# Kernel optimization log

Hardware: AMD Instinct MI355X
Metric: run time of the kernel (lower is better)

Reference implementation:

```python
import jax, jax.numpy as jnp
import numpy as np

N = 50000
E = 800000
D_IN = 128
D_HID = 128
D_OUT = 64
BN_EPS = 1e-5


def setup_inputs() -> dict:
    key = jax.random.key(0)
    ks = jax.random.split(key, 16)
    s = lambda k, shp, fan: jax.random.normal(k, shp, dtype=jnp.float32) / np.sqrt(fan)
    return {
        "x": jax.random.normal(ks[0], (N, D_IN), dtype=jnp.float32),
        "edge_index": jax.random.randint(ks[1], (2, E), 0, N, dtype=jnp.int64),
        # layer 1: SAGEConv(in -> hid)
        "w1l": s(ks[2], (D_IN, D_HID), D_IN),
        "w1r": s(ks[3], (D_IN, D_HID), D_IN),
        "b1": jnp.zeros((D_HID,), jnp.float32),
        "g1": jnp.ones((D_HID,), jnp.float32),
        "be1": jnp.zeros((D_HID,), jnp.float32),
        # layer 2: SAGEConv(hid -> hid)
        "w2l": s(ks[4], (D_HID, D_HID), D_HID),
        "w2r": s(ks[5], (D_HID, D_HID), D_HID),
        "b2": jnp.zeros((D_HID,), jnp.float32),
        "g2": jnp.ones((D_HID,), jnp.float32),
        "be2": jnp.zeros((D_HID,), jnp.float32),
        # layer 3: SAGEConv(hid -> out)
        "w3l": s(ks[6], (D_HID, D_OUT), D_HID),
        "w3r": s(ks[7], (D_HID, D_OUT), D_HID),
        "b3": jnp.zeros((D_OUT,), jnp.float32),
    }


def sage_conv(x, src, dst, wl, wr, b):
    # mean aggregation of source-node features onto destination nodes
    msg_sum = jax.ops.segment_sum(x[src], dst, num_segments=N)  # [N, d]
    deg = jax.ops.segment_sum(jnp.ones((src.shape[0],), x.dtype), dst, num_segments=N)
    mean = msg_sum / jnp.maximum(deg, 1.0)[:, None]
    return mean @ wl + x @ wr + b


def batch_norm(x, g, b):
    mu = jnp.mean(x, axis=0)
    var = jnp.var(x, axis=0)
    return (x - mu) * jax.lax.rsqrt(var + BN_EPS) * g + b


def reference(x, edge_index, w1l, w1r, b1, g1, be1, w2l, w2r, b2, g2, be2, w3l, w3r, b3):
    src, dst = edge_index[0], edge_index[1]
    h = sage_conv(x, src, dst, w1l, w1r, b1)
    h = jax.nn.relu(batch_norm(h, g1, be1))
    h = sage_conv(h, src, dst, w2l, w2r, b2)
    h = jax.nn.relu(batch_norm(h, g2, be2))
    return sage_conv(h, src, dst, w3l, w3r, b3)
```

## Files before the change

### kernel.cpp

```cpp
#include <hip/hip_runtime.h>
#include <hip/hip_bf16.h>

#define NN 50000
#define NE 800000
#define DH 128
#define NB1 196
#define NBK 391
#define EPB 4096

typedef __attribute__((ext_vector_type(8))) short bf16x8;
typedef __attribute__((ext_vector_type(4))) float f32x4;
typedef __attribute__((ext_vector_type(8))) unsigned short us8;
typedef __attribute__((ext_vector_type(4))) unsigned short us4;

__device__ __forceinline__ unsigned short f2bf(float f) {
  unsigned int u = __builtin_bit_cast(unsigned int, f);
  unsigned int r = (u + 0x7FFFu + ((u >> 16) & 1u)) >> 16;
  return (unsigned short)r;
}
__device__ __forceinline__ float bf2f(unsigned int h16) {
  unsigned int u = h16 << 16;
  return __builtin_bit_cast(float, u);
}

__global__ void k_cvt_x(const float* __restrict__ x, unsigned short* __restrict__ xb, int n8) {
  int i = blockIdx.x * blockDim.x + threadIdx.x;
  if (i >= n8) return;
  const float4* p = reinterpret_cast<const float4*>(x) + (size_t)i * 2;
  float4 a = p[0], b = p[1];
  us8 o;
  o[0] = f2bf(a.x); o[1] = f2bf(a.y); o[2] = f2bf(a.z); o[3] = f2bf(a.w);
  o[4] = f2bf(b.x); o[5] = f2bf(b.y); o[6] = f2bf(b.z); o[7] = f2bf(b.w);
  reinterpret_cast<us8*>(xb)[i] = o;
}

__global__ void k_prep_w(const float* __restrict__ wl, const float* __restrict__ wr,
                         unsigned short* __restrict__ wt, int dout) {
  int idx = blockIdx.x * blockDim.x + threadIdx.x;
  if (idx >= dout * 256) return;
  int c = idx >> 8, k = idx & 255;
  float v = (k < DH) ? wl[k * dout + c] : wr[(k - DH) * dout + c];
  wt[idx] = f2bf(v);
}

__global__ void k_prep_w3(const float* __restrict__ w3l, const float* __restrict__ w3r,
                          unsigned short* __restrict__ wt) {
  int idx = blockIdx.x * blockDim.x + threadIdx.x;
  if (idx >= 128 * 128) return;
  int c = idx >> 7, k = idx & 127;
  float v = (c < 64) ? w3l[k * 64 + c] : w3r[k * 64 + (c - 64)];
  wt[idx] = f2bf(v);
}

__global__ void k_deg(const int* __restrict__ dst, int* __restrict__ deg) {
  int e = blockIdx.x * blockDim.x + threadIdx.x;
  if (e < NE) atomicAdd(&deg[dst[e]], 1);
}

__global__ void k_scan1(const int* __restrict__ deg, int* __restrict__ iscan,
                        int* __restrict__ bsum) {
  __shared__ int s[256];
  int t = threadIdx.x;
  int i = blockIdx.x * 256 + t;
  int d = (i < NN) ? deg[i] : 0;
  s[t] = d;
  __syncthreads();
  for (int off = 1; off < 256; off <<= 1) {
    int v = (t >= off) ? s[t - off] : 0;
    __syncthreads();
    s[t] += v;
    __syncthreads();
  }
  if (i < NN) iscan[i] = s[t];
  if (t == 255) bsum[blockIdx.x] = s[255];
}

__global__ void k_scan2(int* __restrict__ bsum) {
  __shared__ int s[256];
  int t = threadIdx.x;
  int v = (t < NB1) ? bsum[t] : 0;
  s[t] = v;
  __syncthreads();
  for (int off = 1; off < 256; off <<= 1) {
    int u = (t >= off) ? s[t - off] : 0;
    __syncthreads();
    s[t] += u;
    __syncthreads();
  }
  if (t < NB1) bsum[t] = s[t] - v;
}

__global__ void k_scan3(const int* __restrict__ deg, const int* __restrict__ iscan,
                        const int* __restrict__ bsum, int* __restrict__ rowptr,
                        int* __restrict__ bcursor, float* __restrict__ invd) {
  int i = blockIdx.x * 256 + threadIdx.x;
  if (i >= NN) return;
  int d = deg[i];
  int excl = bsum[blockIdx.x] + iscan[i] - d;
  rowptr[i] = excl;
  if ((i & 127) == 0) bcursor[i >> 7] = excl;
  invd[i] = 1.0f / (float)(d > 0 ? d : 1);
  if (i == 0) rowptr[NN] = NE;
}

__global__ __launch_bounds__(256) void k_bucket(const int* __restrict__ src,
                                                const int* __restrict__ dst,
                                                int* __restrict__ bcursor,
                                                int2* __restrict__ ebuf) {
  __shared__ int lcnt[NBK], lbase[NBK];
  int t = threadIdx.x;
  for (int b = t; b < NBK; b += 256) lcnt[b] = 0;
  __syncthreads();
  int base = blockIdx.x * EPB;
  int d[16], s[16];
#pragma unroll
  for (int i = 0; i < 16; ++i) {
    int e = base + i * 256 + t;
    if (e < NE) { d[i] = dst[e]; s[i] = src[e]; }
    else d[i] = -1;
  }
#pragma unroll
  for (int i = 0; i < 16; ++i)
    if (d[i] >= 0) atomicAdd(&lcnt[d[i] >> 7], 1);
  __syncthreads();
  for (int b = t; b < NBK; b += 256) {
    int c = lcnt[b];
    lbase[b] = c > 0 ? atomicAdd(&bcursor[b], c) : 0;
    lcnt[b] = 0;
  }
  __syncthreads();
#pragma unroll
  for (int i = 0; i < 16; ++i) {
    if (d[i] >= 0) {
      int b = d[i] >> 7;
      int r = atomicAdd(&lcnt[b], 1);
      ebuf[lbase[b] + r] = make_int2(s[i], d[i]);
    }
  }
}

__global__ __launch_bounds__(256) void k_fill2(const int* __restrict__ rowptr,
                                               const int2* __restrict__ ebuf,
                                               int* __restrict__ adj) {
  int b = blockIdx.x;
  int n0 = b << 7;
  int n1 = n0 + 128; if (n1 > NN) n1 = NN;
  __shared__ int cur[128];
  int t = threadIdx.x;
  if (t < n1 - n0) cur[t] = rowptr[n0 + t];
  __syncthreads();
  int e0 = rowptr[n0], e1 = rowptr[n1];
  for (int e = e0 + t; e < e1; e += 256) {
    int2 pr = ebuf[e];
    int p = atomicAdd(&cur[pr.y - n0], 1);
    adj[p] = pr.x;
  }
}

__global__ __launch_bounds__(256) void k_agg(const unsigned short* __restrict__ h,
                                             const int* __restrict__ rowptr,
                                             const int* __restrict__ adj,
                                             const float* __restrict__ invd,
                                             unsigned short* __restrict__ meanb) {
  int wid = (blockIdx.x * blockDim.x + threadIdx.x) >> 6;
  int lane = threadIdx.x & 63;
  if (wid >= NN) return;
  int lo = rowptr[wid], hi = rowptr[wid + 1];
  int q = lane >> 4;
  int c = (lane & 15) << 3;
  float a[8] = {};
  int e = lo;
#pragma unroll 2
  for (; e + 4 <= hi; e += 4) {
    int s = adj[e + q];
    us8 v = *reinterpret_cast<const us8*>(h + (size_t)s * DH + c);
#pragma unroll
    for (int j = 0; j < 8; ++j) a[j] += bf2f(v[j]);
  }
  if (q < hi - e) {
    int s = adj[e + q];
    us8 v = *reinterpret_cast<const us8*>(h + (size_t)s * DH + c);
#pragma unroll
    for (int j = 0; j < 8; ++j) a[j] += bf2f(v[j]);
  }
#pragma unroll
  for (int j = 0; j < 8; ++j) {
    a[j] += __shfl_xor(a[j], 16);
    a[j] += __shfl_xor(a[j], 32);
  }
  if (q == 0) {
    float iv = invd[wid];
    us8 o;
#pragma unroll
    for (int j = 0; j < 8; ++j) o[j] = f2bf(a[j] * iv);
    *reinterpret_cast<us8*>(meanb + (size_t)wid * DH + c) = o;
  }
}

__global__ __launch_bounds__(256) void k_agg3(const unsigned short* __restrict__ t3,
                                              const int* __restrict__ rowptr,
                                              const int* __restrict__ adj,
                                              const float* __restrict__ invd,
                                              const float* __restrict__ b3,
                                              float* __restrict__ out) {
  int wid = (blockIdx.x * blockDim.x + threadIdx.x) >> 6;
  int lane = threadIdx.x & 63;
  if (wid >= NN) return;
  int lo = rowptr[wid], hi = rowptr[wid + 1];
  int q = lane >> 4;
  int c = (lane & 15) << 2;
  float a[4] = {};
  int e = lo;
#pragma unroll 2
  for (; e + 4 <= hi; e += 4) {
    int s = adj[e + q];
    us4 v = *reinterpret_cast<const us4*>(t3 + (size_t)s * 128 + c);
#pragma unroll
    for (int j = 0; j < 4; ++j) a[j] += bf2f(v[j]);
  }
  if (q < hi - e) {
    int s = adj[e + q];
    us4 v = *reinterpret_cast<const us4*>(t3 + (size_t)s * 128 + c);
#pragma unroll
    for (int j = 0; j < 4; ++j) a[j] += bf2f(v[j]);
  }
#pragma unroll
  for (int j = 0; j < 4; ++j) {
    a[j] += __shfl_xor(a[j], 16);
    a[j] += __shfl_xor(a[j], 32);
  }
  if (q == 0) {
    float iv = invd[wid];
    us4 w = *reinterpret_cast<const us4*>(t3 + (size_t)wid * 128 + 64 + c);
    float4 o;
    o.x = a[0] * iv + bf2f(w[0]) + b3[c + 0];
    o.y = a[1] * iv + bf2f(w[1]) + b3[c + 1];
    o.z = a[2] * iv + bf2f(w[2]) + b3[c + 2];
    o.w = a[3] * iv + bf2f(w[3]) + b3[c + 3];
    *reinterpret_cast<float4*>(out + (size_t)wid * 64 + c) = o;
  }
}

template <bool SPLIT, bool STATS>
__global__ __launch_bounds__(256) void k_gemm(const unsigned short* __restrict__ Am,
                                              const unsigned short* __restrict__ Ah,
                                              const unsigned short* __restrict__ Wt,
                                              const float* __restrict__ bias,
                                              unsigned short* __restrict__ outb,
                                              float* __restrict__ stats) {
  constexpr int KS = SPLIT ? 8 : 4;
  constexpr int WK = KS * 32;
  int lane = threadIdx.x & 63;
  int w = threadIdx.x >> 6;
  int wr = w >> 1, wc = w & 1;
  int rowbase = blockIdx.x * 128 + wr * 64;
  int colbase = wc * 64;
  int lr = lane & 15, lk = (lane >> 4) << 3;

  f32x4 acc[4][4] = {};
#pragma unroll
  for (int ks = 0; ks < KS; ++ks) {
    const unsigned short* Ab = (!SPLIT || ks < 4) ? Am : Ah;
    int ka = ((ks & 3) << 5) + lk;
    int kw = (ks << 5) + lk;
    bf16x8 af[4], bfr[4];
#pragma unroll
    for (int i = 0; i < 4; ++i) {
      int r = rowbase + i * 16 + lr;
      r = r < NN ? r : NN - 1;
      af[i] = *reinterpret_cast<const bf16x8*>(Ab + (size_t)r * DH + ka);
    }
#pragma unroll
    for (int j = 0; j < 4; ++j)
      bfr[j] = *reinterpret_cast<const bf16x8*>(Wt + (size_t)(colbase + j * 16 + lr) * WK + kw);
#pragma unroll
    for (int i = 0; i < 4; ++i)
#pragma unroll
      for (int j = 0; j < 4; ++j)
        acc[i][j] = __builtin_amdgcn_mfma_f32_16x16x32_bf16(af[i], bfr[j], acc[i][j], 0, 0, 0);
  }

  float bv[4];
#pragma unroll
  for (int j = 0; j < 4; ++j) bv[j] = bias ? bias[colbase + j * 16 + lr] : 0.0f;

  float s1[4] = {}, s2[4] = {};
#pragma unroll
  for (int i = 0; i < 4; ++i) {
#pragma unroll
    for (int j = 0; j < 4; ++j) {
      int col = colbase + j * 16 + lr;
#pragma unroll
      for (int r = 0; r < 4; ++r) {
        int row = rowbase + i * 16 + ((lane >> 4) << 2) + r;
        if (row < NN) {
          float val = acc[i][j][r] + bv[j];
          outb[(size_t)row * 128 + col] = f2bf(val);
          if (STATS) { s1[j] += val; s2[j] += val * val; }
        }
      }
    }
  }

  if (STATS) {
    __shared__ float sd[2][128][2];
#pragma unroll
    for (int j = 0; j < 4; ++j) {
      s1[j] += __shfl_xor(s1[j], 16);
      s1[j] += __shfl_xor(s1[j], 32);
      s2[j] += __shfl_xor(s2[j], 16);
      s2[j] += __shfl_xor(s2[j], 32);
    }
    if (lane < 16) {
#pragma unroll
      for (int j = 0; j < 4; ++j) {
        sd[wr][colbase + j * 16 + lane][0] = s1[j];
        sd[wr][colbase + j * 16 + lane][1] = s2[j];
      }
    }
    __syncthreads();
    int t = threadIdx.x;
    if (t < 128) {
      atomicAdd(&stats[t], sd[0][t][0] + sd[1][t][0]);
      atomicAdd(&stats[128 + t], sd[0][t][1] + sd[1][t][1]);
    }
  }
}

__global__ void k_bnapply(const unsigned short* __restrict__ gin, const float* __restrict__ stats,
                          const float* __restrict__ g, const float* __restrict__ be,
                          unsigned short* __restrict__ hb) {
  int i = blockIdx.x * blockDim.x + threadIdx.x;
  if (i >= NN * DH / 8) return;
  int c = (i * 8) & 127;
  us8 v = reinterpret_cast<const us8*>(gin)[i];
  us8 o;
#pragma unroll
  for (int j = 0; j < 8; ++j) {
    int col = c + j;
    float mu = stats[col] * (1.0f / NN);
    float var = stats[128 + col] * (1.0f / NN) - mu * mu;
    float rs = rsqrtf(var + 1e-5f);
    float val = (bf2f(v[j]) - mu) * rs * g[col] + be[col];
    o[j] = f2bf(fmaxf(val, 0.0f));
  }
  reinterpret_cast<us8*>(hb)[i] = o;
}

extern "C" void kernel_launch(void* const* d_in, const int* in_sizes, int n_in,
                              void* d_out, int out_size, void* d_ws, size_t ws_size,
                              hipStream_t stream) {
  const float* x = (const float*)d_in[0];
  const int* ei = (const int*)d_in[1];
  const int* srcp = ei;
  const int* dstp = ei + NE;
  const float* w1l = (const float*)d_in[2];
  const float* w1r = (const float*)d_in[3];
  const float* b1 = (const float*)d_in[4];
  const float* g1 = (const float*)d_in[5];
  const float* be1 = (const float*)d_in[6];
  const float* w2l = (const float*)d_in[7];
  const float* w2r = (const float*)d_in[8];
  const float* b2 = (const float*)d_in[9];
  const float* g2 = (const float*)d_in[10];
  const float* be2 = (const float*)d_in[11];
  const float* w3l = (const float*)d_in[12];
  const float* w3r = (const float*)d_in[13];
  const float* b3 = (const float*)d_in[14];

  char* ws = (char*)d_ws;
  size_t off = 0;
  auto alloc = [&](size_t bytes) {
    char* p = ws + off;
    off = (off + bytes + 255) & ~(size_t)255;
    return p;
  };
  unsigned short* xb = (unsigned short*)alloc((size_t)NN * DH * 2);
  unsigned short* h1 = (unsigned short*)alloc((size_t)NN * DH * 2);
  unsigned short* h2 = (unsigned short*)alloc((size_t)NN * DH * 2);
  unsigned short* meanb = (unsigned short*)alloc((size_t)NN * DH * 2);
  unsigned short* gbuf = (unsigned short*)alloc((size_t)NN * DH * 2);
  unsigned short* w1t = (unsigned short*)alloc(128 * 256 * 2);
  unsigned short* w2t = (unsigned short*)alloc(128 * 256 * 2);
  unsigned short* w3t = (unsigned short*)alloc(128 * 128 * 2);
  int* deg = (int*)alloc(NN * 4);
  int* rowptr = (int*)alloc((NN + 1) * 4);
  int* adj = (int*)alloc((size_t)NE * 4);
  int2* ebuf = (int2*)alloc((size_t)NE * 8);
  int* bcursor = (int*)alloc(NBK * 4);
  float* invd = (float*)alloc(NN * 4);
  float* stats1 = (float*)alloc(2 * DH * 4);
  float* stats2 = (float*)alloc(2 * DH * 4);
  int* iscan = (int*)alloc(NN * 4);
  int* bsum = (int*)alloc(NB1 * 4);

  hipMemsetAsync(deg, 0, NN * 4, stream);
  hipMemsetAsync(stats1, 0, 2 * 2 * DH * 4 + 256, stream);
  k_cvt_x<<<(NN * DH / 8 + 255) / 256, 256, 0, stream>>>(x, xb, NN * DH / 8);
  k_prep_w<<<128, 256, 0, stream>>>(w1l, w1r, w1t, 128);
  k_prep_w<<<128, 256, 0, stream>>>(w2l, w2r, w2t, 128);
  k_prep_w3<<<64, 256, 0, stream>>>(w3l, w3r, w3t);
  k_deg<<<(NE + 255) / 256, 256, 0, stream>>>(dstp, deg);
  k_scan1<<<NB1, 256, 0, stream>>>(deg, iscan, bsum);
  k_scan2<<<1, 256, 0, stream>>>(bsum);
  k_scan3<<<NB1, 256, 0, stream>>>(deg, iscan, bsum, rowptr, bcursor, invd);
  k_bucket<<<(NE + EPB - 1) / EPB, 256, 0, stream>>>(srcp, dstp, bcursor, ebuf);
  k_fill2<<<NBK, 256, 0, stream>>>(rowptr, ebuf, adj);

  int agg_blocks = (NN * 64 + 255) / 256;
  int gemm_blocks = (NN + 127) / 128;

  k_agg<<<agg_blocks, 256, 0, stream>>>(xb, rowptr, adj, invd, meanb);
  k_gemm<true, true><<<gemm_blocks, 256, 0, stream>>>(meanb, xb, w1t, b1, gbuf, stats1);
  k_bnapply<<<(NN * DH / 8 + 255) / 256, 256, 0, stream>>>(gbuf, stats1, g1, be1, h1);

  k_agg<<<agg_blocks, 256, 0, stream>>>(h1, rowptr, adj, invd, meanb);
  k_gemm<true, true><<<gemm_blocks, 256, 0, stream>>>(meanb, h1, w2t, b2, gbuf, stats2);
  k_bnapply<<<(NN * DH / 8 + 255) / 256, 256, 0, stream>>>(gbuf, stats2, g2, be2, h2);

  k_gemm<false, false><<<gemm_blocks, 256, 0, stream>>>(h2, nullptr, w3t, nullptr, gbuf, nullptr);
  k_agg3<<<agg_blocks, 256, 0, stream>>>(gbuf, rowptr, adj, invd, b3, (float*)d_out);
}
```

Baseline: 269.2 us.

## Fuse BN-apply into aggregation/GEMM loads and merge prep and degree passes

```diff
diff --git a/kernel.cpp b/kernel.cpp
--- a/kernel.cpp
+++ b/kernel.cpp
@@ -7,6 +7,7 @@
 #define NB1 196
 #define NBK 391
 #define EPB 4096
+#define CAPB 4096
 
 typedef __attribute__((ext_vector_type(8))) short bf16x8;
 typedef __attribute__((ext_vector_type(4))) float f32x4;
@@ -23,38 +24,77 @@
   return __builtin_bit_cast(float, u);
 }
 
-__global__ void k_cvt_x(const float* __restrict__ x, unsigned short* __restrict__ xb, int n8) {
-  int i = blockIdx.x * blockDim.x + threadIdx.x;
-  if (i >= n8) return;
-  const float4* p = reinterpret_cast<const float4*>(x) + (size_t)i * 2;
-  float4 a = p[0], b = p[1];
-  us8 o;
-  o[0] = f2bf(a.x); o[1] = f2bf(a.y); o[2] = f2bf(a.z); o[3] = f2bf(a.w);
-  o[4] = f2bf(b.x); o[5] = f2bf(b.y); o[6] = f2bf(b.z); o[7] = f2bf(b.w);
-  reinterpret_cast<us8*>(xb)[i] = o;
-}
-
-__global__ void k_prep_w(const float* __restrict__ wl, const float* __restrict__ wr,
-                         unsigned short* __restrict__ wt, int dout) {
-  int idx = blockIdx.x * blockDim.x + threadIdx.x;
-  if (idx >= dout * 256) return;
-  int c = idx >> 8, k = idx & 255;
-  float v = (k < DH) ? wl[k * dout + c] : wr[(k - DH) * dout + c];
-  wt[idx] = f2bf(v);
-}
-
-__global__ void k_prep_w3(const float* __restrict__ w3l, const float* __restrict__ w3r,
-                          unsigned short* __restrict__ wt) {
-  int idx = blockIdx.x * blockDim.x + threadIdx.x;
-  if (idx >= 128 * 128) return;
-  int c = idx >> 7, k = idx & 127;
-  float v = (c < 64) ? w3l[k * 64 + c] : w3r[k * 64 + (c - 64)];
-  wt[idx] = f2bf(v);
-}
-
-__global__ void k_deg(const int* __restrict__ dst, int* __restrict__ deg) {
-  int e = blockIdx.x * blockDim.x + threadIdx.x;
-  if (e < NE) atomicAdd(&deg[dst[e]], 1);
+__global__ __launch_bounds__(256) void k_prep(const float* __restrict__ x,
+                                              const float* __restrict__ w1l, const float* __restrict__ w1r,
+                                              const float* __restrict__ w2l, const float* __restrict__ w2r,
+                                              const float* __restrict__ w3l, const float* __restrict__ w3r,
+                                              unsigned short* __restrict__ xb,
+                                              unsigned short* __restrict__ w1t,
+                                              unsigned short* __restrict__ w2t,
+                                              unsigned short* __restrict__ w3t) {
+  int b = blockIdx.x, t = threadIdx.x;
+  if (b < 3125) {
+    int i = b * 256 + t;
+    const float4* p = reinterpret_cast<const float4*>(x) + (size_t)i * 2;
+    float4 a = p[0], bb = p[1];
+    us8 o;
+    o[0] = f2bf(a.x); o[1] = f2bf(a.y); o[2] = f2bf(a.z); o[3] = f2bf(a.w);
+    o[4] = f2bf(bb.x); o[5] = f2bf(bb.y); o[6] = f2bf(bb.z); o[7] = f2bf(bb.w);
+    reinterpret_cast<us8*>(xb)[i] = o;
+  } else if (b < 3381) {
+    bool is1 = b < 3253;
+    int idx = (b - (is1 ? 3125 : 3253)) * 256 + t;
+    int c = idx >> 8, k = idx & 255;
+    const float* wl = is1 ? w1l : w2l;
+    const float* wr = is1 ? w1r : w2r;
+    float v = (k < DH) ? wl[k * DH + c] : wr[(k - DH) * DH + c];
+    (is1 ? w1t : w2t)[idx] = f2bf(v);
+  } else {
+    int idx = (b - 3381) * 256 + t;
+    int c = idx >> 7, k = idx & 127;
+    float v = (c < 64) ? w3l[k * 64 + c] : w3r[k * 64 + (c - 64)];
+    w3t[idx] = f2bf(v);
+  }
+}
+
+__global__ __launch_bounds__(256) void k_bucket(const int* __restrict__ src,
+                                                const int* __restrict__ dst,
+                                                int* __restrict__ deg,
+                                                int* __restrict__ bcnt,
+                                                int* __restrict__ ebuf) {
+  __shared__ int lcnt[NBK], lbase[NBK];
+  int t = threadIdx.x;
+  for (int b = t; b < NBK; b += 256) lcnt[b] = 0;
+  __syncthreads();
+  int base = blockIdx.x * EPB;
+  int d[16], s[16];
+#pragma unroll
+  for (int i = 0; i < 16; ++i) {
+    int e = base + i * 256 + t;
+    if (e < NE) { d[i] = dst[e]; s[i] = src[e]; }
+    else d[i] = -1;
+  }
+#pragma unroll
+  for (int i = 0; i < 16; ++i)
+    if (d[i] >= 0) {
+      atomicAdd(&deg[d[i]], 1);
+      atomicAdd(&lcnt[d[i] >> 7], 1);
+    }
+  __syncthreads();
+  for (int b = t; b < NBK; b += 256) {
+    int c = lcnt[b];
+    lbase[b] = c > 0 ? atomicAdd(&bcnt[b], c) : 0;
+    lcnt[b] = 0;
+  }
+  __syncthreads();
+#pragma unroll
+  for (int i = 0; i < 16; ++i) {
+    if (d[i] >= 0) {
+      int b = d[i] >> 7;
+      int r = atomicAdd(&lcnt[b], 1);
+      ebuf[(size_t)b * CAPB + lbase[b] + r] = s[i] | ((d[i] & 127) << 20);
+    }
+  }
 }
 
 __global__ void k_scan1(const int* __restrict__ deg, int* __restrict__ iscan,
@@ -92,55 +132,19 @@
 
 __global__ void k_scan3(const int* __restrict__ deg, const int* __restrict__ iscan,
                         const int* __restrict__ bsum, int* __restrict__ rowptr,
-                        int* __restrict__ bcursor, float* __restrict__ invd) {
+                        float* __restrict__ invd) {
   int i = blockIdx.x * 256 + threadIdx.x;
   if (i >= NN) return;
   int d = deg[i];
   int excl = bsum[blockIdx.x] + iscan[i] - d;
   rowptr[i] = excl;
-  if ((i & 127) == 0) bcursor[i >> 7] = excl;
   invd[i] = 1.0f / (float)(d > 0 ? d : 1);
   if (i == 0) rowptr[NN] = NE;
 }
 
-__global__ __launch_bounds__(256) void k_bucket(const int* __restrict__ src,
-                                                const int* __restrict__ dst,
-                                                int* __restrict__ bcursor,
-                                                int2* __restrict__ ebuf) {
-  __shared__ int lcnt[NBK], lbase[NBK];
-  int t = threadIdx.x;
-  for (int b = t; b < NBK; b += 256) lcnt[b] = 0;
-  __syncthreads();
-  int base = blockIdx.x * EPB;
-  int d[16], s[16];
-#pragma unroll
-  for (int i = 0; i < 16; ++i) {
-    int e = base + i * 256 + t;
-    if (e < NE) { d[i] = dst[e]; s[i] = src[e]; }
-    else d[i] = -1;
-  }
-#pragma unroll
-  for (int i = 0; i < 16; ++i)
-    if (d[i] >= 0) atomicAdd(&lcnt[d[i] >> 7], 1);
-  __syncthreads();
-  for (int b = t; b < NBK; b += 256) {
-    int c = lcnt[b];
-    lbase[b] = c > 0 ? atomicAdd(&bcursor[b], c) : 0;
-    lcnt[b] = 0;
-  }
-  __syncthreads();
-#pragma unroll
-  for (int i = 0; i < 16; ++i) {
-    if (d[i] >= 0) {
-      int b = d[i] >> 7;
-      int r = atomicAdd(&lcnt[b], 1);
-      ebuf[lbase[b] + r] = make_int2(s[i], d[i]);
-    }
-  }
-}
-
 __global__ __launch_bounds__(256) void k_fill2(const int* __restrict__ rowptr,
-                                               const int2* __restrict__ ebuf,
+                                               const int* __restrict__ bcnt,
+                                               const int* __restrict__ ebuf,
                                                int* __restrict__ adj) {
   int b = blockIdx.x;
   int n0 = b << 7;
@@ -149,18 +153,23 @@
   int t = threadIdx.x;
   if (t < n1 - n0) cur[t] = rowptr[n0 + t];
   __syncthreads();
-  int e0 = rowptr[n0], e1 = rowptr[n1];
-  for (int e = e0 + t; e < e1; e += 256) {
-    int2 pr = ebuf[e];
-    int p = atomicAdd(&cur[pr.y - n0], 1);
-    adj[p] = pr.x;
-  }
-}
-
+  int cnt = bcnt[b];
+  const int* eb = ebuf + (size_t)b * CAPB;
+  for (int e = t; e < cnt; e += 256) {
+    int p = eb[e];
+    int pos = atomicAdd(&cur[(p >> 20) & 127], 1);
+    adj[pos] = p & 0xFFFFF;
+  }
+}
+
+template <bool BNA>
 __global__ __launch_bounds__(256) void k_agg(const unsigned short* __restrict__ h,
                                              const int* __restrict__ rowptr,
                                              const int* __restrict__ adj,
                                              const float* __restrict__ invd,
+                                             const float* __restrict__ stats,
+                                             const float* __restrict__ g,
+                                             const float* __restrict__ be,
                                              unsigned short* __restrict__ meanb) {
   int wid = (blockIdx.x * blockDim.x + threadIdx.x) >> 6;
   int lane = threadIdx.x & 63;
@@ -168,6 +177,18 @@
   int lo = rowptr[wid], hi = rowptr[wid + 1];
   int q = lane >> 4;
   int c = (lane & 15) << 3;
+  float sc[8], sh[8];
+  if (BNA) {
+#pragma unroll
+    for (int j = 0; j < 8; ++j) {
+      int col = c + j;
+      float mu = stats[col] * (1.0f / NN);
+      float var = stats[128 + col] * (1.0f / NN) - mu * mu;
+      float rs = rsqrtf(var + 1e-5f);
+      sc[j] = rs * g[col];
+      sh[j] = be[col] - mu * sc[j];
+    }
+  }
   float a[8] = {};
   int e = lo;
 #pragma unroll 2
@@ -175,13 +196,19 @@
     int s = adj[e + q];
     us8 v = *reinterpret_cast<const us8*>(h + (size_t)s * DH + c);
 #pragma unroll
-    for (int j = 0; j < 8; ++j) a[j] += bf2f(v[j]);
+    for (int j = 0; j < 8; ++j) {
+      float f = bf2f(v[j]);
+      a[j] += BNA ? fmaxf(f * sc[j] + sh[j], 0.0f) : f;
+    }
   }
   if (q < hi - e) {
     int s = adj[e + q];
     us8 v = *reinterpret_cast<const us8*>(h + (size_t)s * DH + c);
 #pragma unroll
-    for (int j = 0; j < 8; ++j) a[j] += bf2f(v[j]);
+    for (int j = 0; j < 8; ++j) {
+      float f = bf2f(v[j]);
+      a[j] += BNA ? fmaxf(f * sc[j] + sh[j], 0.0f) : f;
+    }
   }
 #pragma unroll
   for (int j = 0; j < 8; ++j) {
@@ -241,15 +268,31 @@
   }
 }
 
-template <bool SPLIT, bool STATS>
+template <bool SPLIT, bool STATS, bool APPLY>
 __global__ __launch_bounds__(256) void k_gemm(const unsigned short* __restrict__ Am,
                                               const unsigned short* __restrict__ Ah,
                                               const unsigned short* __restrict__ Wt,
                                               const float* __restrict__ bias,
+                                              const float* __restrict__ stA,
+                                              const float* __restrict__ gA,
+                                              const float* __restrict__ beA,
                                               unsigned short* __restrict__ outb,
                                               float* __restrict__ stats) {
   constexpr int KS = SPLIT ? 8 : 4;
   constexpr int WK = KS * 32;
+  __shared__ float asc[DH], ash[DH];
+  if (APPLY) {
+    int t = threadIdx.x;
+    if (t < DH) {
+      float mu = stA[t] * (1.0f / NN);
+      float var = stA[128 + t] * (1.0f / NN) - mu * mu;
+      float rs = rsqrtf(var + 1e-5f);
+      float scv = rs * gA[t];
+      asc[t] = scv;
+      ash[t] = beA[t] - mu * scv;
+    }
+    __syncthreads();
+  }
   int lane = threadIdx.x & 63;
   int w = threadIdx.x >> 6;
   int wr = w >> 1, wc = w & 1;
@@ -261,6 +304,7 @@
 #pragma unroll
   for (int ks = 0; ks < KS; ++ks) {
     const unsigned short* Ab = (!SPLIT || ks < 4) ? Am : Ah;
+    bool tr = APPLY && (!SPLIT || ks >= 4);
     int ka = ((ks & 3) << 5) + lk;
     int kw = (ks << 5) + lk;
     bf16x8 af[4], bfr[4];
@@ -268,7 +312,18 @@
     for (int i = 0; i < 4; ++i) {
       int r = rowbase + i * 16 + lr;
       r = r < NN ? r : NN - 1;
-      af[i] = *reinterpret_cast<const bf16x8*>(Ab + (size_t)r * DH + ka);
+      us8 raw = *reinterpret_cast<const us8*>(Ab + (size_t)r * DH + ka);
+      if (tr) {
+        us8 o;
+#pragma unroll
+        for (int j = 0; j < 8; ++j) {
+          float f = bf2f(raw[j]);
+          o[j] = f2bf(fmaxf(f * asc[ka + j] + ash[ka + j], 0.0f));
+        }
+        af[i] = __builtin_bit_cast(bf16x8, o);
+      } else {
+        af[i] = __builtin_bit_cast(bf16x8, raw);
+      }
     }
 #pragma unroll
     for (int j = 0; j < 4; ++j)
@@ -325,26 +380,6 @@
       atomicAdd(&stats[128 + t], sd[0][t][1] + sd[1][t][1]);
     }
   }
-}
-
-__global__ void k_bnapply(const unsigned short* __restrict__ gin, const float* __restrict__ stats,
-                          const float* __restrict__ g, const float* __restrict__ be,
-                          unsigned short* __restrict__ hb) {
-  int i = blockIdx.x * blockDim.x + threadIdx.x;
-  if (i >= NN * DH / 8) return;
-  int c = (i * 8) & 127;
-  us8 v = reinterpret_cast<const us8*>(gin)[i];
-  us8 o;
-#pragma unroll
-  for (int j = 0; j < 8; ++j) {
-    int col = c + j;
-    float mu = stats[col] * (1.0f / NN);
-    float var = stats[128 + col] * (1.0f / NN) - mu * mu;
-    float rs = rsqrtf(var + 1e-5f);
-    float val = (bf2f(v[j]) - mu) * rs * g[col] + be[col];
-    o[j] = f2bf(fmaxf(val, 0.0f));
-  }
-  reinterpret_cast<us8*>(hb)[i] = o;
 }
 
 extern "C" void kernel_launch(void* const* d_in, const int* in_sizes, int n_in,
@@ -376,48 +411,44 @@
     return p;
   };
   unsigned short* xb = (unsigned short*)alloc((size_t)NN * DH * 2);
-  unsigned short* h1 = (unsigned short*)alloc((size_t)NN * DH * 2);
-  unsigned short* h2 = (unsigned short*)alloc((size_t)NN * DH * 2);
   unsigned short* meanb = (unsigned short*)alloc((size_t)NN * DH * 2);
-  unsigned short* gbuf = (unsigned short*)alloc((size_t)NN * DH * 2);
+  unsigned short* gbuf1 = (unsigned short*)alloc((size_t)NN * DH * 2);
+  unsigned short* gbuf2 = (unsigned short*)alloc((size_t)NN * DH * 2);
   unsigned short* w1t = (unsigned short*)alloc(128 * 256 * 2);
   unsigned short* w2t = (unsigned short*)alloc(128 * 256 * 2);
   unsigned short* w3t = (unsigned short*)alloc(128 * 128 * 2);
   int* deg = (int*)alloc(NN * 4);
+  int* bcnt = (int*)alloc(NBK * 4);
+  float* stats1 = (float*)alloc(2 * DH * 4);
+  float* stats2 = (float*)alloc(2 * DH * 4);
+  size_t zlen = (char*)(stats2 + 2 * DH) - (char*)deg;
   int* rowptr = (int*)alloc((NN + 1) * 4);
   int* adj = (int*)alloc((size_t)NE * 4);
-  int2* ebuf = (int2*)alloc((size_t)NE * 8);
-  int* bcursor = (int*)alloc(NBK * 4);
+  int* ebuf = (int*)alloc((size_t)NBK * CAPB * 4);
   float* invd = (float*)alloc(NN * 4);
-  float* stats1 = (float*)alloc(2 * DH * 4);
-  float* stats2 = (float*)alloc(2 * DH * 4);
   int* iscan = (int*)alloc(NN * 4);
   int* bsum = (int*)alloc(NB1 * 4);
 
-  hipMemsetAsync(deg, 0, NN * 4, stream);
-  hipMemsetAsync(stats1, 0, 2 * 2 * DH * 4 + 256, stream);
-  k_cvt_x<<<(NN * DH / 8 + 255) / 256, 256, 0, stream>>>(x, xb, NN * DH / 8);
-  k_prep_w<<<128, 256, 0, stream>>>(w1l, w1r, w1t, 128);
-  k_prep_w<<<128, 256, 0, stream>>>(w2l, w2r, w2t, 128);
-  k_prep_w3<<<64, 256, 0, stream>>>(w3l, w3r, w3t);
-  k_deg<<<(NE + 255) / 256, 256, 0, stream>>>(dstp, deg);
+  hipMemsetAsync(deg, 0, zlen, stream);
+  k_prep<<<3445, 256, 0, stream>>>(x, w1l, w1r, w2l, w2r, w3l, w3r, xb, w1t, w2t, w3t);
+  k_bucket<<<(NE + EPB - 1) / EPB, 256, 0, stream>>>(srcp, dstp, deg, bcnt, ebuf);
   k_scan1<<<NB1, 256, 0, stream>>>(deg, iscan, bsum);
   k_scan2<<<1, 256, 0, stream>>>(bsum);
-  k_scan3<<<NB1, 256, 0, stream>>>(deg, iscan, bsum, rowptr, bcursor, invd);
-  k_bucket<<<(NE + EPB - 1) / EPB, 256, 0, stream>>>(srcp, dstp, bcursor, ebuf);
-  k_fill2<<<NBK, 256, 0, stream>>>(rowptr, ebuf, adj);
+  k_scan3<<<NB1, 256, 0, stream>>>(deg, iscan, bsum, rowptr, invd);
+  k_fill2<<<NBK, 256, 0, stream>>>(rowptr, bcnt, ebuf, adj);
 
   int agg_blocks = (NN * 64 + 255) / 256;
   int gemm_blocks = (NN + 127) / 128;
 
-  k_agg<<<agg_blocks, 256, 0, stream>>>(xb, rowptr, adj, invd, meanb);
-  k_gemm<true, true><<<gemm_blocks, 256, 0, stream>>>(meanb, xb, w1t, b1, gbuf, stats1);
-  k_bnapply<<<(NN * DH / 8 + 255) / 256, 256, 0, stream>>>(gbuf, stats1, g1, be1, h1);
-
-  k_agg<<<agg_blocks, 256, 0, stream>>>(h1, rowptr, adj, invd, meanb);
-  k_gemm<true, true><<<gemm_blocks, 256, 0, stream>>>(meanb, h1, w2t, b2, gbuf, stats2);
-  k_bnapply<<<(NN * DH / 8 + 255) / 256, 256, 0, stream>>>(gbuf, stats2, g2, be2, h2);
-
-  k_gemm<false, false><<<gemm_blocks, 256, 0, stream>>>(h2, nullptr, w3t, nullptr, gbuf, nullptr);
-  k_agg3<<<agg_blocks, 256, 0, stream>>>(gbuf, rowptr, adj, invd, b3, (float*)d_out);
-}
+  k_agg<false><<<agg_blocks, 256, 0, stream>>>(xb, rowptr, adj, invd, nullptr, nullptr, nullptr, meanb);
+  k_gemm<true, true, false><<<gemm_blocks, 256, 0, stream>>>(
+      meanb, xb, w1t, b1, nullptr, nullptr, nullptr, gbuf1, stats1);
+
+  k_agg<true><<<agg_blocks, 256, 0, stream>>>(gbuf1, rowptr, adj, invd, stats1, g1, be1, meanb);
+  k_gemm<true, true, true><<<gemm_blocks, 256, 0, stream>>>(
+      meanb, gbuf1, w2t, b2, stats1, g1, be1, gbuf2, stats2);
+
+  k_gemm<false, false, true><<<gemm_blocks, 256, 0, stream>>>(
+      gbuf2, nullptr, w3t, nullptr, stats2, g2, be2, gbuf1, nullptr);
+  k_agg3<<<agg_blocks, 256, 0, stream>>>(gbuf1, rowptr, adj, invd, b3, (float*)d_out);
+}
```

Result: faster. 245.8 us (-8.7%).
